# Kernel optimization log

Measured on AMD Instinct MI355X. Metric: run time of the kernel, lower is better.

The kernel has to match this reference:

```python
import jax, jax.numpy as jnp
import numpy as np

B, S, D_MODEL, H = 2, 2048, 1024, 16
HD = D_MODEL // H  # head_dim = 64


def setup_inputs() -> dict:
    key = jax.random.key(0)
    kx, kq, kk, kv, ko = jax.random.split(key, 5)
    scale = 1.0 / np.sqrt(D_MODEL)
    return {
        "x": jax.random.normal(kx, (B, S, D_MODEL), dtype=jnp.float32),
        "Wq": jax.random.normal(kq, (D_MODEL, D_MODEL), dtype=jnp.float32) * scale,
        "Wk": jax.random.normal(kk, (D_MODEL, D_MODEL), dtype=jnp.float32) * scale,
        "Wv": jax.random.normal(kv, (D_MODEL, D_MODEL), dtype=jnp.float32) * scale,
        "Wo": jax.random.normal(ko, (D_MODEL, D_MODEL), dtype=jnp.float32) * scale,
        "bo": jnp.zeros((D_MODEL,), dtype=jnp.float32),
    }


def reference(x, Wq, Wk, Wv, Wo, bo):
    b, s, _ = x.shape
    # project and split heads: [b, h, s, hd]
    q = (x @ Wq).reshape(b, s, H, HD).transpose(0, 2, 1, 3)
    k = (x @ Wk).reshape(b, s, H, HD).transpose(0, 2, 1, 3)
    v = (x @ Wv).reshape(b, s, H, HD).transpose(0, 2, 1, 3)
    # full attn score materialization, as in the original module
    scores = jnp.einsum("bhqd,bhkd->bhqk", q, k)
    causal = jnp.triu(jnp.ones((s, s), dtype=bool), k=1)  # True above diagonal -> masked
    scores = jnp.where(causal, -jnp.inf, scores)
    attn = jax.nn.softmax(scores / np.sqrt(HD), axis=-1)  # dropout p=0.0 (eval)
    ctx = jnp.einsum("bhqk,bhkd->bqhd", attn, v).reshape(b, s, D_MODEL)
    return ctx @ Wo + bo
```

## Files before the change

### kernel.cpp

```cpp
#include <hip/hip_runtime.h>
#include <stdint.h>

typedef __bf16 bf16x8 __attribute__((ext_vector_type(8)));
typedef float f32x4 __attribute__((ext_vector_type(4)));

static constexpr int B_ = 2, S_ = 2048, D_ = 1024, H_ = 16, HD_ = 64;
static constexpr int M_ = B_ * S_;
static constexpr size_t HSZ = (size_t)B_ * H_ * S_ * HD_;

#define DEV_INLINE __device__ __forceinline__

#define SC2F (0.125f * 1.4426950408889634f)

DEV_INLINE uint16_t f2bf(float f) {
  __bf16 h = (__bf16)f;
  return __builtin_bit_cast(uint16_t, h);
}
DEV_INLINE float fmax3(float a, float b, float c) { return fmaxf(fmaxf(a, b), c); }

#define GLD16(gptr, lptr)                                                        \
  __builtin_amdgcn_global_load_lds(                                              \
      (const __attribute__((address_space(1))) void*)(gptr),                     \
      (__attribute__((address_space(3))) void*)(lptr), 16, 0, 0)

__global__ void cvt_x_kernel(const float* __restrict__ x, uint16_t* __restrict__ xb) {
  int i = blockIdx.x * 256 + threadIdx.x;
  float4 v = reinterpret_cast<const float4*>(x)[i];
  ushort4 o;
  o.x = f2bf(v.x); o.y = f2bf(v.y); o.z = f2bf(v.z); o.w = f2bf(v.w);
  reinterpret_cast<ushort4*>(xb)[i] = o;
}

__global__ void tr_w_kernel(const float* __restrict__ W0, const float* __restrict__ W1,
                            const float* __restrict__ W2, const float* __restrict__ W3,
                            uint16_t* __restrict__ Wt) {
  __shared__ float tile[32][33];
  const float* W = (blockIdx.z == 0) ? W0 : (blockIdx.z == 1) ? W1
                   : (blockIdx.z == 2) ? W2 : W3;
  uint16_t* dst = Wt + (size_t)blockIdx.z * D_ * D_;
  int c = blockIdx.x * 32 + threadIdx.x;
  int r0 = blockIdx.y * 32;
#pragma unroll
  for (int j = threadIdx.y; j < 32; j += 8)
    tile[j][threadIdx.x] = W[(size_t)(r0 + j) * D_ + c];
  __syncthreads();
  int oc = blockIdx.y * 32 + threadIdx.x;
  int or0 = blockIdx.x * 32;
#pragma unroll
  for (int j = threadIdx.y; j < 32; j += 8)
    dst[(size_t)(or0 + j) * D_ + oc] = f2bf(tile[threadIdx.x][j]);
}

template <int EPI>
__global__ __launch_bounds__(256, 2)
void gemm_bt_kernel(const uint16_t* __restrict__ A, const uint16_t* __restrict__ Bt,
                    uint16_t* __restrict__ Cb, float* __restrict__ Cf,
                    const float* __restrict__ bias, int K, int gx, int chunk) {
  __shared__ uint16_t lds[2][2][128 * 32];
  const int tid = threadIdx.x;
  const int lane = tid & 63;
  const int wid = tid >> 6;
  const int lo = lane & 15, hi = lane >> 4;

  const int id = blockIdx.x;
  const int tilei = (id & 7) * chunk + (id >> 3);
  const int bx = tilei % gx, by = tilei / gx;
  const int row0 = by * 128, col0 = bx * 128;
  const int wr = (wid >> 1) * 64, wc = (wid & 1) * 64;

  const uint16_t* gA = A + (size_t)(row0 + (tid >> 2)) * K + (tid & 3) * 8;
  const uint16_t* gB = Bt + (size_t)(col0 + (tid >> 2)) * K + (tid & 3) * 8;

  f32x4 acc[4][4] = {};

  auto stage = [&](int kt, int buf) {
    const uint16_t* a = gA + kt * 32;
    const uint16_t* b = gB + kt * 32;
    char* la = (char*)&lds[buf][0][0] + tid * 16;
    char* lb = (char*)&lds[buf][1][0] + tid * 16;
    GLD16(a, la);
    GLD16(a + (size_t)64 * K, la + 4096);
    GLD16(b, lb);
    GLD16(b + (size_t)64 * K, lb + 4096);
  };

  const int nk = K >> 5;
  stage(0, 0);
  __syncthreads();
  for (int kt = 0; kt < nk; ++kt) {
    const int cur = kt & 1;
    if (kt + 1 < nk) stage(kt + 1, cur ^ 1);
    const uint16_t* lA = &lds[cur][0][0];
    const uint16_t* lB = &lds[cur][1][0];
    bf16x8 af[4], bfr[4];
#pragma unroll
    for (int m = 0; m < 4; ++m)
      af[m] = *(const bf16x8*)(lA + (wr + m * 16 + lo) * 32 + hi * 8);
#pragma unroll
    for (int n = 0; n < 4; ++n)
      bfr[n] = *(const bf16x8*)(lB + (wc + n * 16 + lo) * 32 + hi * 8);
    __builtin_amdgcn_s_setprio(1);
#pragma unroll
    for (int m = 0; m < 4; ++m)
#pragma unroll
      for (int n = 0; n < 4; ++n)
        acc[m][n] = __builtin_amdgcn_mfma_f32_16x16x32_bf16(af[m], bfr[n], acc[m][n], 0, 0, 0);
    __builtin_amdgcn_s_setprio(0);
    __syncthreads();
  }

#pragma unroll
  for (int m = 0; m < 4; ++m)
#pragma unroll
    for (int n = 0; n < 4; ++n) {
      const int gr0 = row0 + wr + m * 16 + hi * 4;
      const int gc = col0 + wc + n * 16 + lo;
      if (EPI == 0) {
        const int which = gc >> 10, c = gc & 1023;
        const int hh = c >> 6, d = c & 63;
        const int bb = gr0 >> 11, s0 = gr0 & 2047;
        if (which == 2) {
          ushort4 pk;
          pk.x = f2bf(acc[m][n][0]); pk.y = f2bf(acc[m][n][1]);
          pk.z = f2bf(acc[m][n][2]); pk.w = f2bf(acc[m][n][3]);
          *reinterpret_cast<ushort4*>(
              &Cb[2 * HSZ + ((size_t)(bb * H_ + hh) * HD_ + d) * S_ + s0]) = pk;
        } else {
          const float qs = (which == 0) ? SC2F : 1.0f;
#pragma unroll
          for (int j = 0; j < 4; ++j)
            Cb[(size_t)which * HSZ + (((size_t)(bb * H_ + hh) * S_ + s0 + j) * HD_ + d)] =
                f2bf(acc[m][n][j] * qs);
        }
      } else {
#pragma unroll
        for (int j = 0; j < 4; ++j)
          Cf[(size_t)(gr0 + j) * D_ + gc] = acc[m][n][j] + bias[gc];
      }
    }
}

__global__ __launch_bounds__(256, 2)
void attn_kernel(const uint16_t* __restrict__ QKV, uint16_t* __restrict__ ctx) {
  __shared__ uint16_t ldsKV[3][2][4096];
  __shared__ uint16_t ldsP[64][72];

  const int tid = threadIdx.x;
  const int lane = tid & 63;
  const int w = tid >> 6;
  const int lo = lane & 15, hi = lane >> 4;
  const int swz = (hi * 8) ^ ((lo & 6) << 2);

  const int g = blockIdx.x;
  const int p = g >> 5;
  const int bh = g & 31;
  const int h = bh & 15, b = bh >> 4;

  const size_t bhs = ((size_t)(b * H_ + h)) * S_ * HD_;
  const uint16_t* Q  = QKV + bhs;
  const uint16_t* Kp = QKV + HSZ + bhs;
  const uint16_t* Vt = QKV + 2 * HSZ + bhs;

  bf16x8 ones;
#pragma unroll
  for (int e = 0; e < 8; ++e) ones[e] = __builtin_bit_cast(__bf16, (uint16_t)0x3F80);

  const int srow = tid >> 2;
  const int scol = ((tid & 3) ^ ((tid >> 3) & 3)) * 8;
  auto stage = [&](int kt, int bufi) {
    const uint16_t* gk = Kp + (size_t)(kt * 64 + srow) * HD_ + scol;
    char* lk = (char*)&ldsKV[bufi][0][0] + tid * 16;
    GLD16(gk, lk);
    GLD16(gk + 32, lk + 4096);
    const uint16_t* gv = Vt + (size_t)srow * S_ + kt * 64 + scol;
    char* lv = (char*)&ldsKV[bufi][1][0] + tid * 16;
    GLD16(gv, lv);
    GLD16(gv + 32, lv + 4096);
  };

  auto sweep = [&](int qt, int nkv) {
    const int q0w = qt * 64 + w * 16;
    const int qg = q0w + lo;
    bf16x8 qf[2];
#pragma unroll
    for (int ks = 0; ks < 2; ++ks)
      qf[ks] = *(const bf16x8*)(Q + (size_t)qg * HD_ + ks * 32 + hi * 8);

    f32x4 acco[4] = {};
    f32x4 lacc = {};
    float mstate = -1e30f;

    stage(0, 0);
    if (1 < nkv) stage(1, 1);
    asm volatile("s_waitcnt vmcnt(4)" ::: "memory");
    __builtin_amdgcn_s_barrier();
    __builtin_amdgcn_sched_barrier(0);

    for (int kt = 0; kt < nkv; ++kt) {
      const int buf = kt % 3;
      const bool staged = (kt + 2 < nkv);
      if (staged) stage(kt + 2, (kt + 2) % 3);

      const uint16_t* lK = &ldsKV[buf][0][0];
      bf16x8 ak[4][2];
#pragma unroll
      for (int n = 0; n < 4; ++n)
#pragma unroll
        for (int ks = 0; ks < 2; ++ks)
          ak[n][ks] = *(const bf16x8*)(lK + ks * 2048 + (n * 16 + lo) * 32 + swz);

      f32x4 st[4];
      __builtin_amdgcn_s_setprio(1);
#pragma unroll
      for (int n = 0; n < 4; ++n) {
        f32x4 z = {};
        z = __builtin_amdgcn_mfma_f32_16x16x32_bf16(ak[n][0], qf[0], z, 0, 0, 0);
        st[n] = __builtin_amdgcn_mfma_f32_16x16x32_bf16(ak[n][1], qf[1], z, 0, 0, 0);
      }
      __builtin_amdgcn_s_setprio(0);

      if (kt == nkv - 1) {
#pragma unroll
        for (int n = 0; n < 4; ++n)
#pragma unroll
          for (int j = 0; j < 4; ++j) {
            int kvg = kt * 64 + n * 16 + hi * 4 + j;
            if (kvg > qg) st[n][j] = -1e30f;
          }
      }

      float t0 = fmax3(st[0][0], st[0][1], st[0][2]);
      float t1 = fmax3(t0, st[0][3], st[1][0]);
      float t2 = fmax3(t1, st[1][1], st[1][2]);
      float t3 = fmax3(t2, st[1][3], st[2][0]);
      float t4 = fmax3(t3, st[2][1], st[2][2]);
      float t5 = fmax3(t4, st[2][3], st[3][0]);
      float t6 = fmax3(t5, st[3][1], st[3][2]);
      float vmax = fmaxf(t6, st[3][3]);
      vmax = fmaxf(vmax, __shfl_xor(vmax, 16));
      vmax = fmaxf(vmax, __shfl_xor(vmax, 32));

      if (__any(vmax > mstate + 8.f)) {
        float mnew = fmaxf(mstate, vmax);
        float sc = exp2f(mstate - mnew);
        mstate = mnew;
        lacc *= sc;
#pragma unroll
        for (int nd = 0; nd < 4; ++nd)
#pragma unroll
          for (int j = 0; j < 4; ++j) acco[nd][j] *= sc;
      }

#pragma unroll
      for (int n = 0; n < 4; ++n) {
        ushort4 pk;
        pk.x = f2bf(exp2f(st[n][0] - mstate));
        pk.y = f2bf(exp2f(st[n][1] - mstate));
        pk.z = f2bf(exp2f(st[n][2] - mstate));
        pk.w = f2bf(exp2f(st[n][3] - mstate));
        *reinterpret_cast<ushort4*>(&ldsP[w * 16 + lo][n * 16 + hi * 4]) = pk;
      }

      const uint16_t* lV = &ldsKV[buf][1][0];
      bf16x8 ap[2], bv[4][2];
#pragma unroll
      for (int ks = 0; ks < 2; ++ks)
        ap[ks] = *(const bf16x8*)(&ldsP[w * 16 + lo][ks * 32 + hi * 8]);
#pragma unroll
      for (int nd = 0; nd < 4; ++nd)
#pragma unroll
        for (int ks = 0; ks < 2; ++ks)
          bv[nd][ks] = *(const bf16x8*)(lV + ks * 2048 + (nd * 16 + lo) * 32 + swz);
      __builtin_amdgcn_s_setprio(1);
      lacc = __builtin_amdgcn_mfma_f32_16x16x32_bf16(ones, ap[0], lacc, 0, 0, 0);
      lacc = __builtin_amdgcn_mfma_f32_16x16x32_bf16(ones, ap[1], lacc, 0, 0, 0);
#pragma unroll
      for (int nd = 0; nd < 4; ++nd) {
        acco[nd] = __builtin_amdgcn_mfma_f32_16x16x32_bf16(bv[nd][0], ap[0], acco[nd], 0, 0, 0);
        acco[nd] = __builtin_amdgcn_mfma_f32_16x16x32_bf16(bv[nd][1], ap[1], acco[nd], 0, 0, 0);
      }
      __builtin_amdgcn_s_setprio(0);

      if (staged) asm volatile("s_waitcnt vmcnt(4)" ::: "memory");
      else        asm volatile("s_waitcnt vmcnt(0)" ::: "memory");
      __builtin_amdgcn_s_barrier();
      __builtin_amdgcn_sched_barrier(0);
    }

    const float inv = 1.f / lacc[0];
    uint16_t* crow = ctx + (size_t)(b * S_ + qg) * D_ + h * HD_;
#pragma unroll
    for (int nd = 0; nd < 4; ++nd) {
      ushort4 pk;
      pk.x = f2bf(acco[nd][0] * inv); pk.y = f2bf(acco[nd][1] * inv);
      pk.z = f2bf(acco[nd][2] * inv); pk.w = f2bf(acco[nd][3] * inv);
      *reinterpret_cast<ushort4*>(crow + nd * 16 + hi * 4) = pk;
    }
  };

  sweep(p, p + 1);
  __syncthreads();
  sweep(31 - p, 32 - p);
}

extern "C" void kernel_launch(void* const* d_in, const int* in_sizes, int n_in,
                              void* d_out, int out_size, void* d_ws, size_t ws_size,
                              hipStream_t stream) {
  (void)in_sizes; (void)n_in; (void)out_size; (void)ws_size;
  const float* x  = (const float*)d_in[0];
  const float* Wq = (const float*)d_in[1];
  const float* Wk = (const float*)d_in[2];
  const float* Wv = (const float*)d_in[3];
  const float* Wo = (const float*)d_in[4];
  const float* bo = (const float*)d_in[5];
  float* out = (float*)d_out;

  uint16_t* ws  = (uint16_t*)d_ws;
  uint16_t* xb  = ws;
  uint16_t* Wt  = xb + (size_t)M_ * D_;
  uint16_t* QKV = Wt + (size_t)4 * D_ * D_;
  uint16_t* ctx = QKV + 3 * HSZ;

  cvt_x_kernel<<<(M_ * D_) / 1024, 256, 0, stream>>>(x, xb);
  tr_w_kernel<<<dim3(32, 32, 4), dim3(32, 8), 0, stream>>>(Wq, Wk, Wv, Wo, Wt);
  gemm_bt_kernel<0><<<768, 256, 0, stream>>>(xb, Wt, QKV, nullptr, nullptr, D_, 24, 96);
  attn_kernel<<<512, 256, 0, stream>>>(QKV, ctx);
  gemm_bt_kernel<1><<<256, 256, 0, stream>>>(ctx, Wt + (size_t)3 * D_ * D_, nullptr, out, bo, D_, 8, 32);
}
```

Baseline: 116.6 us.

## Split long causal query tiles across two blocks and merge partial softmax results

The attention kernel now gives each block a single query tile. The longest tiles (p>=19) have their KV range split into two halves processed by separate blocks, which write unnormalized bf16 partial outputs and (max, sum) pairs. A new merge kernel rescales and combines these partials into ctx. The KV pipeline drops from three buffers to two to allow three blocks per CU, and the output GEMM switches to 64-row tiles with 512 blocks, while the QKV GEMM's launch bound rises to 3. This is meant to balance causal work across more blocks and fill the GPU, at the cost of an extra launch, bf16 rounding of the partials, and reuse of the xb workspace for the partial buffers.

Result: no change. 117.4 us (+0.8%).

```diff
diff --git a/kernel.cpp b/kernel.cpp
--- a/kernel.cpp
+++ b/kernel.cpp
@@ -8,6 +8,9 @@
 static constexpr int M_ = B_ * S_;
 static constexpr size_t HSZ = (size_t)B_ * H_ * S_ * HD_;
 
+static constexpr int PSPLIT = 19;
+static constexpr int NSPLIT = 32 - PSPLIT;
+
 #define DEV_INLINE __device__ __forceinline__
 
 #define SC2F (0.125f * 1.4426950408889634f)
@@ -15,6 +18,10 @@
 DEV_INLINE uint16_t f2bf(float f) {
   __bf16 h = (__bf16)f;
   return __builtin_bit_cast(uint16_t, h);
+}
+DEV_INLINE float bf2f(uint16_t u) {
+  uint32_t x = (uint32_t)u << 16;
+  return __builtin_bit_cast(float, x);
 }
 DEV_INLINE float fmax3(float a, float b, float c) { return fmaxf(fmaxf(a, b), c); }
 
@@ -51,12 +58,14 @@
     dst[(size_t)(or0 + j) * D_ + oc] = f2bf(tile[threadIdx.x][j]);
 }
 
-template <int EPI>
-__global__ __launch_bounds__(256, 2)
+template <int EPI, int BM, int MINW>
+__global__ __launch_bounds__(256, MINW)
 void gemm_bt_kernel(const uint16_t* __restrict__ A, const uint16_t* __restrict__ Bt,
                     uint16_t* __restrict__ Cb, float* __restrict__ Cf,
                     const float* __restrict__ bias, int K, int gx, int chunk) {
-  __shared__ uint16_t lds[2][2][128 * 32];
+  constexpr int MR = BM / 32;
+  __shared__ uint16_t ldsA[2][BM * 32];
+  __shared__ uint16_t ldsB[2][128 * 32];
   const int tid = threadIdx.x;
   const int lane = tid & 63;
   const int wid = tid >> 6;
@@ -65,21 +74,21 @@
   const int id = blockIdx.x;
   const int tilei = (id & 7) * chunk + (id >> 3);
   const int bx = tilei % gx, by = tilei / gx;
-  const int row0 = by * 128, col0 = bx * 128;
-  const int wr = (wid >> 1) * 64, wc = (wid & 1) * 64;
+  const int row0 = by * BM, col0 = bx * 128;
+  const int wr = (wid >> 1) * (BM / 2), wc = (wid & 1) * 64;
 
   const uint16_t* gA = A + (size_t)(row0 + (tid >> 2)) * K + (tid & 3) * 8;
   const uint16_t* gB = Bt + (size_t)(col0 + (tid >> 2)) * K + (tid & 3) * 8;
 
-  f32x4 acc[4][4] = {};
+  f32x4 acc[MR][4] = {};
 
   auto stage = [&](int kt, int buf) {
     const uint16_t* a = gA + kt * 32;
     const uint16_t* b = gB + kt * 32;
-    char* la = (char*)&lds[buf][0][0] + tid * 16;
-    char* lb = (char*)&lds[buf][1][0] + tid * 16;
+    char* la = (char*)&ldsA[buf][0] + tid * 16;
+    char* lb = (char*)&ldsB[buf][0] + tid * 16;
     GLD16(a, la);
-    GLD16(a + (size_t)64 * K, la + 4096);
+    if constexpr (BM == 128) GLD16(a + (size_t)64 * K, la + 4096);
     GLD16(b, lb);
     GLD16(b + (size_t)64 * K, lb + 4096);
   };
@@ -90,18 +99,18 @@
   for (int kt = 0; kt < nk; ++kt) {
     const int cur = kt & 1;
     if (kt + 1 < nk) stage(kt + 1, cur ^ 1);
-    const uint16_t* lA = &lds[cur][0][0];
-    const uint16_t* lB = &lds[cur][1][0];
-    bf16x8 af[4], bfr[4];
-#pragma unroll
-    for (int m = 0; m < 4; ++m)
+    const uint16_t* lA = &ldsA[cur][0];
+    const uint16_t* lB = &ldsB[cur][0];
+    bf16x8 af[MR], bfr[4];
+#pragma unroll
+    for (int m = 0; m < MR; ++m)
       af[m] = *(const bf16x8*)(lA + (wr + m * 16 + lo) * 32 + hi * 8);
 #pragma unroll
     for (int n = 0; n < 4; ++n)
       bfr[n] = *(const bf16x8*)(lB + (wc + n * 16 + lo) * 32 + hi * 8);
     __builtin_amdgcn_s_setprio(1);
 #pragma unroll
-    for (int m = 0; m < 4; ++m)
+    for (int m = 0; m < MR; ++m)
 #pragma unroll
       for (int n = 0; n < 4; ++n)
         acc[m][n] = __builtin_amdgcn_mfma_f32_16x16x32_bf16(af[m], bfr[n], acc[m][n], 0, 0, 0);
@@ -110,7 +119,7 @@
   }
 
 #pragma unroll
-  for (int m = 0; m < 4; ++m)
+  for (int m = 0; m < MR; ++m)
 #pragma unroll
     for (int n = 0; n < 4; ++n) {
       const int gr0 = row0 + wr + m * 16 + hi * 4;
@@ -140,9 +149,10 @@
     }
 }
 
-__global__ __launch_bounds__(256, 2)
-void attn_kernel(const uint16_t* __restrict__ QKV, uint16_t* __restrict__ ctx) {
-  __shared__ uint16_t ldsKV[3][2][4096];
+__global__ __launch_bounds__(256, 3)
+void attn_kernel(const uint16_t* __restrict__ QKV, uint16_t* __restrict__ ctx,
+                 uint16_t* __restrict__ Opart, float2* __restrict__ ml) {
+  __shared__ uint16_t ldsKV[2][2][4096];
   __shared__ uint16_t ldsP[64][72];
 
   const int tid = threadIdx.x;
@@ -152,8 +162,23 @@
   const int swz = (hi * 8) ^ ((lo & 6) << 2);
 
   const int g = blockIdx.x;
-  const int p = g >> 5;
-  const int bh = g & 31;
+  const int bh = g & 31, r = g >> 5;
+  int p, half, k0, k1;
+  bool split;
+  if (r < 2 * NSPLIT) {
+    split = true;
+    p = 31 - (r >> 1);
+    half = r & 1;
+    const int h0 = (p + 2) >> 1;
+    k0 = half ? h0 : 0;
+    k1 = half ? (p + 1) : h0;
+  } else {
+    split = false;
+    p = (31 - NSPLIT) + 2 * NSPLIT - r;
+    half = 0;
+    k0 = 0;
+    k1 = p + 1;
+  }
   const int h = bh & 15, b = bh >> 4;
 
   const size_t bhs = ((size_t)(b * H_ + h)) * S_ * HD_;
@@ -178,115 +203,112 @@
     GLD16(gv + 32, lv + 4096);
   };
 
-  auto sweep = [&](int qt, int nkv) {
-    const int q0w = qt * 64 + w * 16;
-    const int qg = q0w + lo;
-    bf16x8 qf[2];
+  const int q0w = p * 64 + w * 16;
+  const int qg = q0w + lo;
+  bf16x8 qf[2];
+#pragma unroll
+  for (int ks = 0; ks < 2; ++ks)
+    qf[ks] = *(const bf16x8*)(Q + (size_t)qg * HD_ + ks * 32 + hi * 8);
+
+  f32x4 acco[4] = {};
+  f32x4 lacc = {};
+  float mstate = -1e30f;
+
+  stage(k0, k0 & 1);
+  asm volatile("s_waitcnt vmcnt(0)" ::: "memory");
+  __builtin_amdgcn_s_barrier();
+  __builtin_amdgcn_sched_barrier(0);
+
+  for (int kt = k0; kt < k1; ++kt) {
+    const int buf = kt & 1;
+    if (kt + 1 < k1) stage(kt + 1, (kt + 1) & 1);
+
+    const uint16_t* lK = &ldsKV[buf][0][0];
+    bf16x8 ak[4][2];
+#pragma unroll
+    for (int n = 0; n < 4; ++n)
+#pragma unroll
+      for (int ks = 0; ks < 2; ++ks)
+        ak[n][ks] = *(const bf16x8*)(lK + ks * 2048 + (n * 16 + lo) * 32 + swz);
+
+    f32x4 st[4];
+    __builtin_amdgcn_s_setprio(1);
+#pragma unroll
+    for (int n = 0; n < 4; ++n) {
+      f32x4 z = {};
+      z = __builtin_amdgcn_mfma_f32_16x16x32_bf16(ak[n][0], qf[0], z, 0, 0, 0);
+      st[n] = __builtin_amdgcn_mfma_f32_16x16x32_bf16(ak[n][1], qf[1], z, 0, 0, 0);
+    }
+    __builtin_amdgcn_s_setprio(0);
+
+    if (kt == p) {
+#pragma unroll
+      for (int n = 0; n < 4; ++n)
+#pragma unroll
+        for (int j = 0; j < 4; ++j) {
+          int kvg = kt * 64 + n * 16 + hi * 4 + j;
+          if (kvg > qg) st[n][j] = -1e30f;
+        }
+    }
+
+    float t0 = fmax3(st[0][0], st[0][1], st[0][2]);
+    float t1 = fmax3(t0, st[0][3], st[1][0]);
+    float t2 = fmax3(t1, st[1][1], st[1][2]);
+    float t3 = fmax3(t2, st[1][3], st[2][0]);
+    float t4 = fmax3(t3, st[2][1], st[2][2]);
+    float t5 = fmax3(t4, st[2][3], st[3][0]);
+    float t6 = fmax3(t5, st[3][1], st[3][2]);
+    float vmax = fmaxf(t6, st[3][3]);
+    vmax = fmaxf(vmax, __shfl_xor(vmax, 16));
+    vmax = fmaxf(vmax, __shfl_xor(vmax, 32));
+
+    if (__any(vmax > mstate + 8.f)) {
+      float mnew = fmaxf(mstate, vmax);
+      float sc = exp2f(mstate - mnew);
+      mstate = mnew;
+      lacc *= sc;
+#pragma unroll
+      for (int nd = 0; nd < 4; ++nd)
+#pragma unroll
+        for (int j = 0; j < 4; ++j) acco[nd][j] *= sc;
+    }
+
+#pragma unroll
+    for (int n = 0; n < 4; ++n) {
+      ushort4 pk;
+      pk.x = f2bf(exp2f(st[n][0] - mstate));
+      pk.y = f2bf(exp2f(st[n][1] - mstate));
+      pk.z = f2bf(exp2f(st[n][2] - mstate));
+      pk.w = f2bf(exp2f(st[n][3] - mstate));
+      *reinterpret_cast<ushort4*>(&ldsP[w * 16 + lo][n * 16 + hi * 4]) = pk;
+    }
+
+    const uint16_t* lV = &ldsKV[buf][1][0];
+    bf16x8 ap[2], bv[4][2];
 #pragma unroll
     for (int ks = 0; ks < 2; ++ks)
-      qf[ks] = *(const bf16x8*)(Q + (size_t)qg * HD_ + ks * 32 + hi * 8);
-
-    f32x4 acco[4] = {};
-    f32x4 lacc = {};
-    float mstate = -1e30f;
-
-    stage(0, 0);
-    if (1 < nkv) stage(1, 1);
-    asm volatile("s_waitcnt vmcnt(4)" ::: "memory");
+      ap[ks] = *(const bf16x8*)(&ldsP[w * 16 + lo][ks * 32 + hi * 8]);
+#pragma unroll
+    for (int nd = 0; nd < 4; ++nd)
+#pragma unroll
+      for (int ks = 0; ks < 2; ++ks)
+        bv[nd][ks] = *(const bf16x8*)(lV + ks * 2048 + (nd * 16 + lo) * 32 + swz);
+    __builtin_amdgcn_s_setprio(1);
+    lacc = __builtin_amdgcn_mfma_f32_16x16x32_bf16(ones, ap[0], lacc, 0, 0, 0);
+    lacc = __builtin_amdgcn_mfma_f32_16x16x32_bf16(ones, ap[1], lacc, 0, 0, 0);
+#pragma unroll
+    for (int nd = 0; nd < 4; ++nd) {
+      acco[nd] = __builtin_amdgcn_mfma_f32_16x16x32_bf16(bv[nd][0], ap[0], acco[nd], 0, 0, 0);
+      acco[nd] = __builtin_amdgcn_mfma_f32_16x16x32_bf16(bv[nd][1], ap[1], acco[nd], 0, 0, 0);
+    }
+    __builtin_amdgcn_s_setprio(0);
+
+    asm volatile("s_waitcnt vmcnt(0)" ::: "memory");
     __builtin_amdgcn_s_barrier();
     __builtin_amdgcn_sched_barrier(0);
-
-    for (int kt = 0; kt < nkv; ++kt) {
-      const int buf = kt % 3;
-      const bool staged = (kt + 2 < nkv);
-      if (staged) stage(kt + 2, (kt + 2) % 3);
-
-      const uint16_t* lK = &ldsKV[buf][0][0];
-      bf16x8 ak[4][2];
-#pragma unroll
-      for (int n = 0; n < 4; ++n)
-#pragma unroll
-        for (int ks = 0; ks < 2; ++ks)
-          ak[n][ks] = *(const bf16x8*)(lK + ks * 2048 + (n * 16 + lo) * 32 + swz);
-
-      f32x4 st[4];
-      __builtin_amdgcn_s_setprio(1);
-#pragma unroll
-      for (int n = 0; n < 4; ++n) {
-        f32x4 z = {};
-        z = __builtin_amdgcn_mfma_f32_16x16x32_bf16(ak[n][0], qf[0], z, 0, 0, 0);
-        st[n] = __builtin_amdgcn_mfma_f32_16x16x32_bf16(ak[n][1], qf[1], z, 0, 0, 0);
-      }
-      __builtin_amdgcn_s_setprio(0);
-
-      if (kt == nkv - 1) {
-#pragma unroll
-        for (int n = 0; n < 4; ++n)
-#pragma unroll
-          for (int j = 0; j < 4; ++j) {
-            int kvg = kt * 64 + n * 16 + hi * 4 + j;
-            if (kvg > qg) st[n][j] = -1e30f;
-          }
-      }
-
-      float t0 = fmax3(st[0][0], st[0][1], st[0][2]);
-      float t1 = fmax3(t0, st[0][3], st[1][0]);
-      float t2 = fmax3(t1, st[1][1], st[1][2]);
-      float t3 = fmax3(t2, st[1][3], st[2][0]);
-      float t4 = fmax3(t3, st[2][1], st[2][2]);
-      float t5 = fmax3(t4, st[2][3], st[3][0]);
-      float t6 = fmax3(t5, st[3][1], st[3][2]);
-      float vmax = fmaxf(t6, st[3][3]);
-      vmax = fmaxf(vmax, __shfl_xor(vmax, 16));
-      vmax = fmaxf(vmax, __shfl_xor(vmax, 32));
-
-      if (__any(vmax > mstate + 8.f)) {
-        float mnew = fmaxf(mstate, vmax);
-        float sc = exp2f(mstate - mnew);
-        mstate = mnew;
-        lacc *= sc;
-#pragma unroll
-        for (int nd = 0; nd < 4; ++nd)
-#pragma unroll
-          for (int j = 0; j < 4; ++j) acco[nd][j] *= sc;
-      }
-
-#pragma unroll
-      for (int n = 0; n < 4; ++n) {
-        ushort4 pk;
-        pk.x = f2bf(exp2f(st[n][0] - mstate));
-        pk.y = f2bf(exp2f(st[n][1] - mstate));
-        pk.z = f2bf(exp2f(st[n][2] - mstate));
-        pk.w = f2bf(exp2f(st[n][3] - mstate));
-        *reinterpret_cast<ushort4*>(&ldsP[w * 16 + lo][n * 16 + hi * 4]) = pk;
-      }
-
-      const uint16_t* lV = &ldsKV[buf][1][0];
-      bf16x8 ap[2], bv[4][2];
-#pragma unroll
-      for (int ks = 0; ks < 2; ++ks)
-        ap[ks] = *(const bf16x8*)(&ldsP[w * 16 + lo][ks * 32 + hi * 8]);
-#pragma unroll
-      for (int nd = 0; nd < 4; ++nd)
-#pragma unroll
-        for (int ks = 0; ks < 2; ++ks)
-          bv[nd][ks] = *(const bf16x8*)(lV + ks * 2048 + (nd * 16 + lo) * 32 + swz);
-      __builtin_amdgcn_s_setprio(1);
-      lacc = __builtin_amdgcn_mfma_f32_16x16x32_bf16(ones, ap[0], lacc, 0, 0, 0);
-      lacc = __builtin_amdgcn_mfma_f32_16x16x32_bf16(ones, ap[1], lacc, 0, 0, 0);
-#pragma unroll
-      for (int nd = 0; nd < 4; ++nd) {
-        acco[nd] = __builtin_amdgcn_mfma_f32_16x16x32_bf16(bv[nd][0], ap[0], acco[nd], 0, 0, 0);
-        acco[nd] = __builtin_amdgcn_mfma_f32_16x16x32_bf16(bv[nd][1], ap[1], acco[nd], 0, 0, 0);
-      }
-      __builtin_amdgcn_s_setprio(0);
-
-      if (staged) asm volatile("s_waitcnt vmcnt(4)" ::: "memory");
-      else        asm volatile("s_waitcnt vmcnt(0)" ::: "memory");
-      __builtin_amdgcn_s_barrier();
-      __builtin_amdgcn_sched_barrier(0);
-    }
-
+  }
+
+  if (!split) {
     const float inv = 1.f / lacc[0];
     uint16_t* crow = ctx + (size_t)(b * S_ + qg) * D_ + h * HD_;
 #pragma unroll
@@ -296,11 +318,55 @@
       pk.z = f2bf(acco[nd][2] * inv); pk.w = f2bf(acco[nd][3] * inv);
       *reinterpret_cast<ushort4*>(crow + nd * 16 + hi * 4) = pk;
     }
-  };
-
-  sweep(p, p + 1);
-  __syncthreads();
-  sweep(31 - p, 32 - p);
+  } else {
+    const int idx = (bh * NSPLIT + (p - PSPLIT)) * 2 + half;
+    uint16_t* op = Opart + (size_t)idx * 4096;
+    const int qloc = w * 16 + lo;
+#pragma unroll
+    for (int nd = 0; nd < 4; ++nd) {
+      ushort4 pk;
+      pk.x = f2bf(acco[nd][0]); pk.y = f2bf(acco[nd][1]);
+      pk.z = f2bf(acco[nd][2]); pk.w = f2bf(acco[nd][3]);
+      *reinterpret_cast<ushort4*>(op + qloc * 64 + nd * 16 + hi * 4) = pk;
+    }
+    if (hi == 0) ml[idx * 64 + qloc] = make_float2(mstate, lacc[0]);
+  }
+}
+
+__global__ void merge_kernel(const uint16_t* __restrict__ Opart,
+                             const float2* __restrict__ ml,
+                             uint16_t* __restrict__ ctx) {
+  const int t = blockIdx.x;
+  const int bh = t & 31, si = t >> 5;
+  const int h = bh & 15, b = bh >> 4;
+  const int p = PSPLIT + si;
+  const int base = (bh * NSPLIT + si) * 2;
+  const uint16_t* Oa = Opart + (size_t)base * 4096;
+  const uint16_t* Ob = Oa + 4096;
+  const int q = threadIdx.x >> 2, d0 = (threadIdx.x & 3) * 16;
+
+  const float2 A = ml[base * 64 + q];
+  const float2 Bv = ml[(base + 1) * 64 + q];
+  const float m = fmaxf(A.x, Bv.x);
+  float sa = exp2f(A.x - m), sb = exp2f(Bv.x - m);
+  const float inv = 1.f / (A.y * sa + Bv.y * sb);
+  sa *= inv; sb *= inv;
+
+  const int4* pa = (const int4*)(Oa + q * 64 + d0);
+  const int4* pb = (const int4*)(Ob + q * 64 + d0);
+  uint16_t* pc = ctx + ((size_t)(b * S_) + p * 64 + q) * D_ + h * HD_ + d0;
+#pragma unroll
+  for (int hf = 0; hf < 2; ++hf) {
+    int4 va = pa[hf], vb = pb[hf];
+    const uint16_t* ua = (const uint16_t*)&va;
+    const uint16_t* ub = (const uint16_t*)&vb;
+    int4 vo;
+    uint16_t* uo = (uint16_t*)&vo;
+#pragma unroll
+    for (int i = 0; i < 8; ++i)
+      uo[i] = f2bf(bf2f(ua[i]) * sa + bf2f(ub[i]) * sb);
+    *(int4*)(pc + hf * 8) = vo;
+  }
 }
 
 extern "C" void kernel_launch(void* const* d_in, const int* in_sizes, int n_in,
@@ -320,10 +386,13 @@
   uint16_t* Wt  = xb + (size_t)M_ * D_;
   uint16_t* QKV = Wt + (size_t)4 * D_ * D_;
   uint16_t* ctx = QKV + 3 * HSZ;
+  uint16_t* Opart = xb;
+  float2*   mlbuf = (float2*)(xb + (size_t)32 * NSPLIT * 2 * 4096);
 
   cvt_x_kernel<<<(M_ * D_) / 1024, 256, 0, stream>>>(x, xb);
   tr_w_kernel<<<dim3(32, 32, 4), dim3(32, 8), 0, stream>>>(Wq, Wk, Wv, Wo, Wt);
-  gemm_bt_kernel<0><<<768, 256, 0, stream>>>(xb, Wt, QKV, nullptr, nullptr, D_, 24, 96);
-  attn_kernel<<<512, 256, 0, stream>>>(QKV, ctx);
-  gemm_bt_kernel<1><<<256, 256, 0, stream>>>(ctx, Wt + (size_t)3 * D_ * D_, nullptr, out, bo, D_, 8, 32);
-}
+  gemm_bt_kernel<0, 128, 3><<<768, 256, 0, stream>>>(xb, Wt, QKV, nullptr, nullptr, D_, 24, 96);
+  attn_kernel<<<(2 * NSPLIT + PSPLIT) * 32, 256, 0, stream>>>(QKV, ctx, Opart, mlbuf);
+  merge_kernel<<<NSPLIT * 32, 256, 0, stream>>>(Opart, mlbuf, ctx);
+  gemm_bt_kernel<1, 64, 2><<<512, 256, 0, stream>>>(ctx, Wt + (size_t)3 * D_ * D_, nullptr, out, bo, D_, 8, 64);
+}
```
